# Kernel tuning notes

Hardware: AMD Instinct MI355X
Metric: run time of the kernel (lower is better)

The kernel has to match this reference:

```python
import jax, jax.numpy as jnp
import numpy as np

BATCH, OUT_FEATURES = 512, 1024
NUM_BLOCKS, LATTICE_DIM = 32, 4
MAX_INDICES = 256  # q^lattice_dim with q=4, lattice_dim=4


def setup_inputs() -> dict:
    key = jax.random.key(0)
    k1, k2, k3 = jax.random.split(key, 3)
    input_indices = jax.random.randint(k1, (BATCH, NUM_BLOCKS, LATTICE_DIM), 0, MAX_INDICES, dtype=jnp.int64 if jax.config.jax_enable_x64 else jnp.int32)
    weight_indices = jax.random.randint(k2, (OUT_FEATURES, NUM_BLOCKS, LATTICE_DIM), 0, MAX_INDICES, dtype=jnp.int64 if jax.config.jax_enable_x64 else jnp.int32)
    lut_table = jax.random.normal(k3, (MAX_INDICES, MAX_INDICES), dtype=jnp.float32)
    return {"input_indices": input_indices, "weight_indices": weight_indices, "lut_table": lut_table}


def reference(input_indices, weight_indices, lut_table):
    # Flatten block/lattice dims: K = num_blocks * lattice_dim
    B = input_indices.shape[0]
    O = weight_indices.shape[0]
    inp = jnp.clip(input_indices.reshape(B, -1), 0, MAX_INDICES - 1)   # [B, K]
    wgt = jnp.clip(weight_indices.reshape(O, -1), 0, MAX_INDICES - 1)  # [O, K]
    # out[b, o] = sum_k LUT[inp[b, k], wgt[o, k]]
    vals = lut_table[inp[:, None, :], wgt[None, :, :]]  # [B, O, K] gather
    return jnp.sum(vals, axis=-1)  # [B, O]
```

## Files before the change

### kernel.cpp

```cpp
#include <hip/hip_runtime.h>


#define BATCH 512
#define OUTF  1024
#define KDIM  128
#define MIDX  256

typedef _Float16 half4v __attribute__((ext_vector_type(4)));

__global__ __launch_bounds__(1024, 1)
void slt_kernel(const int* __restrict__ inp, const int* __restrict__ wgt,
                const float* __restrict__ lut, float* __restrict__ out) {
    __shared__ __attribute__((aligned(16))) _Float16 lut16[MIDX * MIDX];
    __shared__ __attribute__((aligned(16))) unsigned int i_pack[32 * KDIM / 4];
    __shared__ __attribute__((aligned(16))) unsigned int w_pack[64 * KDIM / 4];

    const int tid   = threadIdx.x;
    const int otile = blockIdx.x;
    const int btile = blockIdx.y;

    const float4* lut4 = (const float4*)lut;
    half4v* l16v = (half4v*)lut16;
    #pragma unroll
    for (int it = 0; it < 16; ++it) {
        int idx = it * 1024 + tid;
        float4 v = lut4[idx];
        half4v h = { (_Float16)v.x, (_Float16)v.y, (_Float16)v.z, (_Float16)v.w };
        l16v[idx] = h;
    }

    {
        int b  = tid >> 5;
        int k4 = tid & 31;
        const int4 iv = *(const int4*)(inp + ((size_t)(btile * 32 + b)) * KDIM + k4 * 4);
        unsigned int w = (unsigned int)(iv.x & 255)
                       | ((unsigned int)(iv.y & 255) << 8)
                       | ((unsigned int)(iv.z & 255) << 16)
                       | ((unsigned int)(iv.w & 255) << 24);
        i_pack[(k4 >> 2) * 128 + b * 4 + (k4 & 3)] = w;
    }
    #pragma unroll
    for (int s = 0; s < 2; ++s) {
        int t2 = tid + s * 1024;
        int o  = t2 >> 5;
        int k4 = t2 & 31;
        const int4 wv = *(const int4*)(wgt + ((size_t)(otile * 64 + o)) * KDIM + k4 * 4);
        unsigned int w = (unsigned int)(wv.x & 255)
                       | ((unsigned int)(wv.y & 255) << 8)
                       | ((unsigned int)(wv.z & 255) << 16)
                       | ((unsigned int)(wv.w & 255) << 24);
        w_pack[(k4 >> 2) * 256 + o * 4 + (k4 & 3)] = w;
    }

    __syncthreads();

    const int bl = tid >> 5;
    const int ol = tid & 31;

    float acc0 = 0.f, acc1 = 0.f;

    for (int k16 = 0; k16 < 8; ++k16) {
        uint4 iw = ((const uint4*)i_pack)[k16 * 32 + bl];
        uint4 wa = ((const uint4*)w_pack)[k16 * 64 + ol];
        uint4 wb = ((const uint4*)w_pack)[k16 * 64 + ol + 32];
        unsigned int ia[4] = { iw.x, iw.y, iw.z, iw.w };
        unsigned int a0[4] = { wa.x, wa.y, wa.z, wa.w };
        unsigned int a1[4] = { wb.x, wb.y, wb.z, wb.w };
        #pragma unroll
        for (int j = 0; j < 4; ++j) {
            #pragma unroll
            for (int jj = 0; jj < 4; ++jj) {
                unsigned int sh  = 8u * jj;
                unsigned int row = ((ia[j] >> sh) & 255u) << 8;
                unsigned int c0  = (a0[j] >> sh) & 255u;
                unsigned int c1  = (a1[j] >> sh) & 255u;
                acc0 += (float)lut16[row + c0];
                acc1 += (float)lut16[row + c1];
            }
        }
    }

    size_t ob = ((size_t)(btile * 32 + bl)) * OUTF + (size_t)(otile * 64) + ol;
    out[ob]      = acc0;
    out[ob + 32] = acc1;
}

extern "C" void kernel_launch(void* const* d_in, const int* in_sizes, int n_in,
                              void* d_out, int out_size, void* d_ws, size_t ws_size,
                              hipStream_t stream) {
    const int*   inp = (const int*)d_in[0];
    const int*   wgt = (const int*)d_in[1];
    const float* lut = (const float*)d_in[2];
    float*       out = (float*)d_out;

    dim3 grid(16, 16);
    dim3 block(1024);
    slt_kernel<<<grid, block, 0, stream>>>(inp, wgt, lut, out);
}
```

Baseline: 72.41 us.

## Retile LUT-gather kernel to wave-uniform input rows with split accumulators

Changes each block's tile from 32 batch rows by 64 output columns to 16 rows by 128 columns. Each 64-lane wavefront now owns one batch row, so the packed input word is read once and made wave-uniform with readfirstlane. Weight indices are stored column-major so consecutive lanes read consecutive LDS words. Two independent accumulator pairs shorten the floating-point dependency chains. The aim is to cut redundant LDS index loads and per-lane row arithmetic, leaving mostly gathers, at the cost of different LDS bank-conflict behavior and a changed grid shape.

```diff
diff --git a/kernel.cpp b/kernel.cpp
--- a/kernel.cpp
+++ b/kernel.cpp
@@ -12,8 +12,8 @@
 void slt_kernel(const int* __restrict__ inp, const int* __restrict__ wgt,
                 const float* __restrict__ lut, float* __restrict__ out) {
     __shared__ __attribute__((aligned(16))) _Float16 lut16[MIDX * MIDX];
-    __shared__ __attribute__((aligned(16))) unsigned int i_pack[32 * KDIM / 4];
-    __shared__ __attribute__((aligned(16))) unsigned int w_pack[64 * KDIM / 4];
+    __shared__ __attribute__((aligned(16))) unsigned int wrow_pack[16 * 32];
+    __shared__ __attribute__((aligned(16))) unsigned int wcol_pack[32 * 128];
 
     const int tid   = threadIdx.x;
     const int otile = blockIdx.x;
@@ -29,60 +29,59 @@
         l16v[idx] = h;
     }
 
+    if (tid < 512) {
+        int b = tid >> 5;
+        int q = tid & 31;
+        const int4 iv = *(const int4*)(inp + ((size_t)(btile * 16 + b)) * KDIM + q * 4);
+        wrow_pack[b * 32 + q] = (unsigned int)(iv.x & 255)
+                              | ((unsigned int)(iv.y & 255) << 8)
+                              | ((unsigned int)(iv.z & 255) << 16)
+                              | ((unsigned int)(iv.w & 255) << 24);
+    }
+
     {
-        int b  = tid >> 5;
-        int k4 = tid & 31;
-        const int4 iv = *(const int4*)(inp + ((size_t)(btile * 32 + b)) * KDIM + k4 * 4);
-        unsigned int w = (unsigned int)(iv.x & 255)
-                       | ((unsigned int)(iv.y & 255) << 8)
-                       | ((unsigned int)(iv.z & 255) << 16)
-                       | ((unsigned int)(iv.w & 255) << 24);
-        i_pack[(k4 >> 2) * 128 + b * 4 + (k4 & 3)] = w;
-    }
-    #pragma unroll
-    for (int s = 0; s < 2; ++s) {
-        int t2 = tid + s * 1024;
-        int o  = t2 >> 5;
-        int k4 = t2 & 31;
-        const int4 wv = *(const int4*)(wgt + ((size_t)(otile * 64 + o)) * KDIM + k4 * 4);
-        unsigned int w = (unsigned int)(wv.x & 255)
-                       | ((unsigned int)(wv.y & 255) << 8)
-                       | ((unsigned int)(wv.z & 255) << 16)
-                       | ((unsigned int)(wv.w & 255) << 24);
-        w_pack[(k4 >> 2) * 256 + o * 4 + (k4 & 3)] = w;
+        int o = tid >> 3;
+        int j = tid & 7;
+        const int* wbase = wgt + ((size_t)(otile * 128 + o)) * KDIM;
+        #pragma unroll
+        for (int i = 0; i < 4; ++i) {
+            int q = j + 8 * i;
+            const int4 wv = *(const int4*)(wbase + q * 4);
+            wcol_pack[q * 128 + o] = (unsigned int)(wv.x & 255)
+                                   | ((unsigned int)(wv.y & 255) << 8)
+                                   | ((unsigned int)(wv.z & 255) << 16)
+                                   | ((unsigned int)(wv.w & 255) << 24);
+        }
     }
 
     __syncthreads();
 
-    const int bl = tid >> 5;
-    const int ol = tid & 31;
+    const int w    = tid >> 6;
+    const int lane = tid & 63;
 
-    float acc0 = 0.f, acc1 = 0.f;
+    float a0 = 0.f, a1 = 0.f, b0 = 0.f, b1 = 0.f;
+    const unsigned int* wr = &wrow_pack[w * 32];
 
-    for (int k16 = 0; k16 < 8; ++k16) {
-        uint4 iw = ((const uint4*)i_pack)[k16 * 32 + bl];
-        uint4 wa = ((const uint4*)w_pack)[k16 * 64 + ol];
-        uint4 wb = ((const uint4*)w_pack)[k16 * 64 + ol + 32];
-        unsigned int ia[4] = { iw.x, iw.y, iw.z, iw.w };
-        unsigned int a0[4] = { wa.x, wa.y, wa.z, wa.w };
-        unsigned int a1[4] = { wb.x, wb.y, wb.z, wb.w };
-        #pragma unroll
-        for (int j = 0; j < 4; ++j) {
-            #pragma unroll
-            for (int jj = 0; jj < 4; ++jj) {
-                unsigned int sh  = 8u * jj;
-                unsigned int row = ((ia[j] >> sh) & 255u) << 8;
-                unsigned int c0  = (a0[j] >> sh) & 255u;
-                unsigned int c1  = (a1[j] >> sh) & 255u;
-                acc0 += (float)lut16[row + c0];
-                acc1 += (float)lut16[row + c1];
-            }
-        }
+    #pragma unroll 4
+    for (int q = 0; q < 32; ++q) {
+        unsigned int rword = __builtin_amdgcn_readfirstlane(wr[q]);
+        unsigned int w0 = wcol_pack[q * 128 + lane];
+        unsigned int w1 = wcol_pack[q * 128 + lane + 64];
+
+        const _Float16* r0 = lut16 + (((rword      ) & 255u) << 8);
+        const _Float16* r1 = lut16 + (((rword >>  8) & 255u) << 8);
+        const _Float16* r2 = lut16 + (((rword >> 16) & 255u) << 8);
+        const _Float16* r3 = lut16 + (((rword >> 24)       ) << 8);
+
+        a0 += (float)r0[(w0      ) & 255u];  a1 += (float)r0[(w1      ) & 255u];
+        b0 += (float)r1[(w0 >>  8) & 255u];  b1 += (float)r1[(w1 >>  8) & 255u];
+        a0 += (float)r2[(w0 >> 16) & 255u];  a1 += (float)r2[(w1 >> 16) & 255u];
+        b0 += (float)r3[(w0 >> 24)        ];  b1 += (float)r3[(w1 >> 24)        ];
     }
 
-    size_t ob = ((size_t)(btile * 32 + bl)) * OUTF + (size_t)(otile * 64) + ol;
-    out[ob]      = acc0;
-    out[ob + 32] = acc1;
+    size_t ob = ((size_t)(btile * 16 + w)) * OUTF + (size_t)(otile * 128) + lane;
+    out[ob]      = a0 + b0;
+    out[ob + 64] = a1 + b1;
 }
 
 extern "C" void kernel_launch(void* const* d_in, const int* in_sizes, int n_in,
@@ -93,7 +92,7 @@
     const float* lut = (const float*)d_in[2];
     float*       out = (float*)d_out;
 
-    dim3 grid(16, 16);
+    dim3 grid(8, 32);
     dim3 block(1024);
     slt_kernel<<<grid, block, 0, stream>>>(inp, wgt, lut, out);
 }
```

After: 73.00 us. About the same (+0.8%).
